# Optimization experiments

Measured on AMD Instinct MI355X. Metric: run time of the kernel, lower is better.

Reference implementation:

```python
import jax, jax.numpy as jnp
import numpy as np

N, H, IN, E = 4096, 64, 64, 10  # notes, hidden, input feat, edge types


def setup_inputs() -> dict:
    key = jax.random.key(0)
    ks = jax.random.split(key, 7)
    std_a = (2.0 / (H + H)) ** 0.5
    std_b = (2.0 / (IN + H)) ** 0.5
    return {
        "input": jax.random.normal(ks[0], (1, N, IN), jnp.float32),
        "hidden": jax.random.normal(ks[1], (1, N, H), jnp.float32),
        # dense per-edge-type adjacency; scaled by 1/N to keep gate pre-activations O(1)
        "edge_matrix": jax.random.uniform(ks[2], (E, N, N), jnp.float32) / N,
        "ba": jnp.zeros((H,), jnp.float32),
        "wz_wr_wh": jax.random.normal(ks[3], (E, H, 3 * H), jnp.float32) * std_a,
        "uz_ur": jax.random.normal(ks[4], (H, 2 * H), jnp.float32) * std_a,
        "uh": jax.random.normal(ks[5], (H, H), jnp.float32) * std_a,
        "input_wzrh": jax.random.normal(ks[6], (IN, 3 * H), jnp.float32) * std_b,
        "iteration": 10,
    }


def reference(input, hidden, edge_matrix, ba, wz_wr_wh, uz_ur, uh, input_wzrh, iteration):
    B, n, _ = input.shape          # B == 1
    h_dim = uh.shape[0]
    n_type = wz_wr_wh.shape[0]
    edge_T = jnp.swapaxes(edge_matrix, 1, 2)          # [E, N, N]
    inp_wzrh = jnp.matmul(input, input_wzrh)          # [B, N, 3H] (loop-invariant)

    def step(h, _):
        # message aggregation per edge type: [E,N,N] @ [B,N,H] -> [E,N,H]
        act = jnp.matmul(edge_T, h) + ba
        # per-edge-type gate projections: [E,N,H] @ [E,H,3H] -> [E,N,3H]
        act_wzrh = jnp.matmul(act, wz_wr_wh) + inp_wzrh
        wz, wr, wh = jnp.split(act_wzrh, 3, axis=-1)
        uz, ur = jnp.split(jnp.matmul(h, uz_ur), 2, axis=-1)  # [B,N,H] each
        z = jax.nn.sigmoid(wz.sum(0) + uz)
        r = jax.nn.sigmoid(wr.sum(0) + ur)
        h_tilde = jnp.tanh(wh.reshape(B, n_type, n, h_dim).sum(1)
                           + jnp.matmul(r * h, uh))
        return (1.0 - z) * h + z * h_tilde, None

    hidden, _ = jax.lax.scan(step, hidden, None, length=iteration)
    return hidden
```

## Files before the change

### kernel.cpp

```cpp
#include <hip/hip_runtime.h>
#include <hip/hip_bf16.h>


typedef __bf16 bf16;
typedef bf16 bf16x8 __attribute__((ext_vector_type(8)));
typedef float f32x4 __attribute__((ext_vector_type(4)));

static_assert(sizeof(bf16) == 2, "bf16 size");

constexpr int kN = 4096;
constexpr int kH = 64;
constexpr int kE = 10;
constexpr int kIter = 10;

constexpr size_t OFF_EDGET = 0;
constexpr size_t SZ_EDGET  = (size_t)kE * kN * kN * 2;
constexpr size_t OFF_HF32  = OFF_EDGET + SZ_EDGET;
constexpr size_t OFF_HBF   = OFF_HF32 + (size_t)kN * kH * 4;
constexpr size_t OFF_HT    = OFF_HBF + (size_t)kN * kH * 2;
constexpr size_t OFF_S     = OFF_HT + (size_t)kN * kH * 2;
constexpr size_t OFF_SBIAS = OFF_S + (size_t)kN * 192 * 4;
constexpr size_t OFF_WT    = OFF_SBIAS + (size_t)kN * 192 * 4;
constexpr size_t OFF_UZT   = OFF_WT + (size_t)kE * 192 * 64 * 2;
constexpr size_t OFF_UHT   = OFF_UZT + (size_t)128 * 64 * 2;
constexpr size_t WS_NEEDED = OFF_UHT + (size_t)64 * 64 * 2;

__device__ __forceinline__ void async16(const void* g, void* l) {
  __builtin_amdgcn_global_load_lds(
      (const __attribute__((address_space(1))) unsigned int*)g,
      (__attribute__((address_space(3))) unsigned int*)l, 16, 0, 0);
}

__device__ __forceinline__ float sigmoidf_(float x) { return 1.0f / (1.0f + __expf(-x)); }
__device__ __forceinline__ float tanhf_(float x) { return 1.0f - 2.0f / (__expf(2.0f * x) + 1.0f); }


__global__ __launch_bounds__(256) void k_transpose(const float* __restrict__ edge,
                                                   bf16* __restrict__ edgeT) {
  const int e = blockIdx.z;
  const int m0 = blockIdx.y * 64;
  const int n0 = blockIdx.x * 64;
  __shared__ bf16 t[64 * 66];
  const float* src = edge + (size_t)e * kN * kN;
  for (int i = threadIdx.x; i < 4096; i += 256) {
    int m = i >> 6, n = i & 63;
    t[n * 66 + m] = (bf16)src[(size_t)(m0 + m) * kN + n0 + n];
  }
  __syncthreads();
  bf16* dst = edgeT + (size_t)e * kN * kN;
  for (int i = threadIdx.x; i < 4096; i += 256) {
    int n = i >> 6, m = i & 63;
    dst[(size_t)(n0 + n) * kN + m0 + m] = t[n * 66 + m];
  }
}

__global__ __launch_bounds__(256) void k_weights(const float* __restrict__ wzwrwh,
                                                 const float* __restrict__ uz_ur,
                                                 const float* __restrict__ uh,
                                                 bf16* __restrict__ WT_all,
                                                 bf16* __restrict__ uzurT,
                                                 bf16* __restrict__ uhT) {
  int idx = blockIdx.x * 256 + threadIdx.x;
  if (idx < kE * 192 * 64) {
    int e = idx / (192 * 64);
    int rem = idx % (192 * 64);
    int c = rem / 64, hh = rem % 64;
    WT_all[idx] = (bf16)wzwrwh[((size_t)e * 64 + hh) * 192 + c];
  }
  if (idx < 128 * 64) {
    int c = idx / 64, hh = idx % 64;
    uzurT[idx] = (bf16)uz_ur[hh * 128 + c];
  }
  if (idx < 64 * 64) {
    int c = idx / 64, hh = idx % 64;
    uhT[idx] = (bf16)uh[hh * 64 + c];
  }
}

__global__ __launch_bounds__(256) void k_hinit(const float* __restrict__ hidden,
                                               float* __restrict__ hf32,
                                               bf16* __restrict__ hbf,
                                               bf16* __restrict__ hT) {
  int idx = blockIdx.x * 256 + threadIdx.x;
  float x = hidden[idx];
  hf32[idx] = x;
  hbf[idx] = (bf16)x;
  int n = idx >> 6, c = idx & 63;
  hT[(size_t)c * kN + n] = (bf16)x;
}

__global__ __launch_bounds__(256) void k_sbias(const float* __restrict__ input,
                                               const float* __restrict__ input_wzrh,
                                               float* __restrict__ SBias,
                                               float* __restrict__ S) {
  int idx = blockIdx.x * 256 + threadIdx.x;
  int n = idx / 192, c = idx % 192;
  float a = 0.f;
#pragma unroll 8
  for (int k = 0; k < 64; k++) a += input[n * 64 + k] * input_wzrh[k * 192 + c];
  a *= (float)kE;
  SBias[idx] = a;
  S[idx] = a;
}

__global__ __launch_bounds__(256) void k_copy(const float* __restrict__ src, float* __restrict__ dst) {
  int idx = blockIdx.x * 256 + threadIdx.x;
  dst[idx] = src[idx];
}

__global__ __launch_bounds__(256, 3) void kA(const bf16* __restrict__ edgeT,
                                             const bf16* __restrict__ hT,
                                             const bf16* __restrict__ WT_all,
                                             const float* __restrict__ ba,
                                             float* __restrict__ S) {
  const int e = blockIdx.y;
  const int n0 = blockIdx.x * 64;
  const int tid = threadIdx.x;
  const int lane = tid & 63;
  const int w = tid >> 6;
  const int l15 = lane & 15;
  const int q = lane >> 4;

  __shared__ bf16 Alds[64 * 64];
  __shared__ bf16 Blds[64 * 64];
  __shared__ bf16 Wlds[192 * 64];
  __shared__ bf16 actlds[64 * 72];

  {
    const int4* src = (const int4*)(WT_all + (size_t)e * 192 * 64);
    int4* dst = (int4*)Wlds;
    for (int i = tid; i < 192 * 64 * 2 / 16; i += 256) dst[i] = src[i];
  }

  f32x4 acc[4] = {};
  const bf16* Abase = edgeT + (size_t)e * kN * kN + (size_t)n0 * kN;

  for (int k0 = 0; k0 < kN; k0 += 64) {
    __syncthreads();
#pragma unroll
    for (int i = 0; i < 2; i++) {
      int c = i * 256 + tid;
      int row = c >> 3, col = (c & 7) * 8;
      async16(Abase + (size_t)row * kN + k0 + col, Alds + c * 8);
    }
#pragma unroll
    for (int i = 0; i < 2; i++) {
      int c = i * 256 + tid;
      int row = c >> 3, col = (c & 7) * 8;
      async16(hT + (size_t)row * kN + k0 + col, Blds + c * 8);
    }
    __syncthreads();
#pragma unroll
    for (int ks = 0; ks < 2; ks++) {
      bf16x8 af = *(const bf16x8*)(Alds + (w * 16 + l15) * 64 + ks * 32 + q * 8);
#pragma unroll
      for (int ct = 0; ct < 4; ct++) {
        bf16x8 bf = *(const bf16x8*)(Blds + (ct * 16 + l15) * 64 + ks * 32 + q * 8);
        acc[ct] = __builtin_amdgcn_mfma_f32_16x16x32_bf16(af, bf, acc[ct], 0, 0, 0);
      }
    }
  }

  __syncthreads();
#pragma unroll
  for (int ct = 0; ct < 4; ct++) {
    int col = ct * 16 + l15;
    float bav = ba[col];
#pragma unroll
    for (int r = 0; r < 4; r++) {
      int row = w * 16 + q * 4 + r;
      actlds[row * 72 + col] = (bf16)(acc[ct][r] + bav);
    }
  }
  __syncthreads();

  f32x4 acc2[12] = {};
#pragma unroll
  for (int ks = 0; ks < 2; ks++) {
    bf16x8 af = *(const bf16x8*)(actlds + (w * 16 + l15) * 72 + ks * 32 + q * 8);
#pragma unroll
    for (int ct = 0; ct < 12; ct++) {
      bf16x8 bf = *(const bf16x8*)(Wlds + (ct * 16 + l15) * 64 + ks * 32 + q * 8);
      acc2[ct] = __builtin_amdgcn_mfma_f32_16x16x32_bf16(af, bf, acc2[ct], 0, 0, 0);
    }
  }
#pragma unroll
  for (int ct = 0; ct < 12; ct++) {
    int col = ct * 16 + l15;
#pragma unroll
    for (int r = 0; r < 4; r++) {
      int row = n0 + w * 16 + q * 4 + r;
      unsafeAtomicAdd(&S[(size_t)row * 192 + col], acc2[ct][r]);
    }
  }
}

__global__ __launch_bounds__(256) void kB(float* __restrict__ S,
                                          const float* __restrict__ SBias,
                                          const bf16* __restrict__ hbf,
                                          const float* __restrict__ hf32,
                                          const bf16* __restrict__ uzurT,
                                          const bf16* __restrict__ uhT,
                                          float* __restrict__ hf32_out,
                                          bf16* __restrict__ hbf_out,
                                          bf16* __restrict__ hT_out,
                                          float* __restrict__ dst) {
  const int n0 = blockIdx.x * 64;
  const int tid = threadIdx.x;
  const int lane = tid & 63;
  const int w = tid >> 6;
  const int l15 = lane & 15;
  const int q = lane >> 4;

  __shared__ bf16 hA[64 * 72];
  __shared__ bf16 uzT[128 * 72];
  __shared__ bf16 uhl[64 * 72];
  __shared__ bf16 rhl[64 * 72];

  for (int i = tid; i < 64 * 8; i += 256) {
    int row = i >> 3, col = (i & 7) * 8;
    *(int4*)(hA + row * 72 + col) = *(const int4*)(hbf + (size_t)(n0 + row) * 64 + col);
  }
  for (int i = tid; i < 128 * 8; i += 256) {
    int row = i >> 3, col = (i & 7) * 8;
    *(int4*)(uzT + row * 72 + col) = *(const int4*)(uzurT + (size_t)row * 64 + col);
  }
  for (int i = tid; i < 64 * 8; i += 256) {
    int row = i >> 3, col = (i & 7) * 8;
    *(int4*)(uhl + row * 72 + col) = *(const int4*)(uhT + (size_t)row * 64 + col);
  }
  __syncthreads();

  f32x4 u[8] = {};
#pragma unroll
  for (int ks = 0; ks < 2; ks++) {
    bf16x8 af = *(const bf16x8*)(hA + (w * 16 + l15) * 72 + ks * 32 + q * 8);
#pragma unroll
    for (int ct = 0; ct < 8; ct++) {
      bf16x8 bf = *(const bf16x8*)(uzT + (ct * 16 + l15) * 72 + ks * 32 + q * 8);
      u[ct] = __builtin_amdgcn_mfma_f32_16x16x32_bf16(af, bf, u[ct], 0, 0, 0);
    }
  }

  float zv[4][4], hv[4][4];
#pragma unroll
  for (int ct = 0; ct < 4; ct++) {
    int col = ct * 16 + l15;
#pragma unroll
    for (int r = 0; r < 4; r++) {
      int row = n0 + w * 16 + q * 4 + r;
      float sz = S[(size_t)row * 192 + col];
      float sr = S[(size_t)row * 192 + 64 + col];
      float z = sigmoidf_(sz + u[ct][r]);
      float rr = sigmoidf_(sr + u[4 + ct][r]);
      float h = hf32[(size_t)row * 64 + col];
      zv[ct][r] = z;
      hv[ct][r] = h;
      rhl[(w * 16 + q * 4 + r) * 72 + col] = (bf16)(rr * h);
    }
  }
  __syncthreads();

  f32x4 t[4] = {};
#pragma unroll
  for (int ks = 0; ks < 2; ks++) {
    bf16x8 af = *(const bf16x8*)(rhl + (w * 16 + l15) * 72 + ks * 32 + q * 8);
#pragma unroll
    for (int ct = 0; ct < 4; ct++) {
      bf16x8 bf = *(const bf16x8*)(uhl + (ct * 16 + l15) * 72 + ks * 32 + q * 8);
      t[ct] = __builtin_amdgcn_mfma_f32_16x16x32_bf16(af, bf, t[ct], 0, 0, 0);
    }
  }

  float hn[4][4];
#pragma unroll
  for (int ct = 0; ct < 4; ct++) {
    int col = ct * 16 + l15;
#pragma unroll
    for (int r = 0; r < 4; r++) {
      int row = n0 + w * 16 + q * 4 + r;
      float wh = S[(size_t)row * 192 + 128 + col];
      float htl = tanhf_(wh + t[ct][r]);
      float z = zv[ct][r];
      float v = (1.0f - z) * hv[ct][r] + z * htl;
      hn[ct][r] = v;
      dst[(size_t)row * 64 + col] = v;
      if (dst != hf32_out) hf32_out[(size_t)row * 64 + col] = v;
      hbf_out[(size_t)row * 64 + col] = (bf16)v;
    }
  }
  __syncthreads();

#pragma unroll
  for (int ct = 0; ct < 4; ct++) {
#pragma unroll
    for (int r = 0; r < 4; r++) {
      int row = w * 16 + q * 4 + r, col = ct * 16 + l15;
      rhl[row * 72 + col] = (bf16)hn[ct][r];
    }
  }
  for (int i = tid; i < 64 * 192; i += 256) S[(size_t)n0 * 192 + i] = SBias[(size_t)n0 * 192 + i];
  __syncthreads();
  for (int i = tid; i < 4096; i += 256) {
    int c = i >> 6, n = i & 63;
    hT_out[(size_t)c * kN + n0 + n] = rhl[n * 72 + c];
  }
}

extern "C" void kernel_launch(void* const* d_in, const int* in_sizes, int n_in,
                              void* d_out, int out_size, void* d_ws, size_t ws_size,
                              hipStream_t stream) {
  const float* input = (const float*)d_in[0];
  const float* hidden = (const float*)d_in[1];
  const float* edge = (const float*)d_in[2];
  const float* ba = (const float*)d_in[3];
  const float* wzwrwh = (const float*)d_in[4];
  const float* uz_ur = (const float*)d_in[5];
  const float* uh = (const float*)d_in[6];
  const float* input_wzrh = (const float*)d_in[7];
  float* out = (float*)d_out;

  if (ws_size < WS_NEEDED) {
    k_copy<<<kN * kH / 256, 256, 0, stream>>>(hidden, out);
    return;
  }

  char* ws = (char*)d_ws;
  bf16* edgeT = (bf16*)(ws + OFF_EDGET);
  float* hf32 = (float*)(ws + OFF_HF32);
  bf16* hbf = (bf16*)(ws + OFF_HBF);
  bf16* hT = (bf16*)(ws + OFF_HT);
  float* S = (float*)(ws + OFF_S);
  float* SBias = (float*)(ws + OFF_SBIAS);
  bf16* WT_all = (bf16*)(ws + OFF_WT);
  bf16* uzurT = (bf16*)(ws + OFF_UZT);
  bf16* uhT = (bf16*)(ws + OFF_UHT);

  k_transpose<<<dim3(kN / 64, kN / 64, kE), 256, 0, stream>>>(edge, edgeT);
  k_weights<<<(kE * 192 * 64) / 256, 256, 0, stream>>>(wzwrwh, uz_ur, uh, WT_all, uzurT, uhT);
  k_hinit<<<(kN * kH) / 256, 256, 0, stream>>>(hidden, hf32, hbf, hT);
  k_sbias<<<(kN * 192) / 256, 256, 0, stream>>>(input, input_wzrh, SBias, S);

  for (int it = 0; it < kIter; it++) {
    kA<<<dim3(kN / 64, kE), 256, 0, stream>>>(edgeT, hT, WT_all, ba, S);
    float* dst = (it == kIter - 1) ? out : hf32;
    kB<<<kN / 64, 256, 0, stream>>>(S, SBias, hbf, hf32, uzurT, uhT, hf32, hbf, hT, dst);
  }
}
```

Baseline: 2.231 ms.

## Double-buffer edge/hidden tiles in kA with XOR-swizzled LDS layout

The main K loop of kA now double-buffers the A (edge) and B (hidden) tiles in LDS, issuing the async loads for the next tile before the MFMAs on the current one. This overlaps global memory traffic with compute and cuts the loop to one barrier per iteration. LDS columns are XOR-swizzled by row to avoid bank conflicts on the bf16x8 reads. The W projection tile is no longer staged in LDS and is read directly from global memory, which frees shared memory for the second buffer but adds uncached-style global reads in the epilogue.

```diff
diff --git a/kernel.cpp b/kernel.cpp
--- a/kernel.cpp
+++ b/kernel.cpp
@@ -121,47 +121,57 @@
   const int l15 = lane & 15;
   const int q = lane >> 4;
 
-  __shared__ bf16 Alds[64 * 64];
-  __shared__ bf16 Blds[64 * 64];
-  __shared__ bf16 Wlds[192 * 64];
+  __shared__ bf16 Alds[2][64 * 64];
+  __shared__ bf16 Blds[2][64 * 64];
   __shared__ bf16 actlds[64 * 72];
 
-  {
-    const int4* src = (const int4*)(WT_all + (size_t)e * 192 * 64);
-    int4* dst = (int4*)Wlds;
-    for (int i = tid; i < 192 * 64 * 2 / 16; i += 256) dst[i] = src[i];
+  const bf16* Abase = edgeT + (size_t)e * kN * kN + (size_t)n0 * kN;
+
+  int srow[2], scol[2];
+#pragma unroll
+  for (int i = 0; i < 2; i++) {
+    int c = i * 256 + tid;
+    srow[i] = c >> 3;
+    scol[i] = ((c & 7) ^ (srow[i] & 7)) * 8;
   }
 
   f32x4 acc[4] = {};
-  const bf16* Abase = edgeT + (size_t)e * kN * kN + (size_t)n0 * kN;
-
+
+#pragma unroll
+  for (int i = 0; i < 2; i++)
+    async16(Abase + (size_t)srow[i] * kN + scol[i], Alds[0] + (i * 256 + tid) * 8);
+#pragma unroll
+  for (int i = 0; i < 2; i++)
+    async16(hT + (size_t)srow[i] * kN + scol[i], Blds[0] + (i * 256 + tid) * 8);
+  __syncthreads();
+
+  int cur = 0;
   for (int k0 = 0; k0 < kN; k0 += 64) {
-    __syncthreads();
-#pragma unroll
-    for (int i = 0; i < 2; i++) {
-      int c = i * 256 + tid;
-      int row = c >> 3, col = (c & 7) * 8;
-      async16(Abase + (size_t)row * kN + k0 + col, Alds + c * 8);
-    }
-#pragma unroll
-    for (int i = 0; i < 2; i++) {
-      int c = i * 256 + tid;
-      int row = c >> 3, col = (c & 7) * 8;
-      async16(hT + (size_t)row * kN + k0 + col, Blds + c * 8);
-    }
-    __syncthreads();
+    if (k0 + 64 < kN) {
+#pragma unroll
+      for (int i = 0; i < 2; i++)
+        async16(Abase + (size_t)srow[i] * kN + (k0 + 64) + scol[i],
+                Alds[cur ^ 1] + (i * 256 + tid) * 8);
+#pragma unroll
+      for (int i = 0; i < 2; i++)
+        async16(hT + (size_t)srow[i] * kN + (k0 + 64) + scol[i],
+                Blds[cur ^ 1] + (i * 256 + tid) * 8);
+    }
 #pragma unroll
     for (int ks = 0; ks < 2; ks++) {
-      bf16x8 af = *(const bf16x8*)(Alds + (w * 16 + l15) * 64 + ks * 32 + q * 8);
+      const int ar = w * 16 + l15;
+      bf16x8 af = *(const bf16x8*)(Alds[cur] + ar * 64 + ((ks * 32 + q * 8) ^ ((ar & 7) << 3)));
 #pragma unroll
       for (int ct = 0; ct < 4; ct++) {
-        bf16x8 bf = *(const bf16x8*)(Blds + (ct * 16 + l15) * 64 + ks * 32 + q * 8);
+        const int br = ct * 16 + l15;
+        bf16x8 bf = *(const bf16x8*)(Blds[cur] + br * 64 + ((ks * 32 + q * 8) ^ ((br & 7) << 3)));
         acc[ct] = __builtin_amdgcn_mfma_f32_16x16x32_bf16(af, bf, acc[ct], 0, 0, 0);
       }
     }
-  }
-
-  __syncthreads();
+    __syncthreads();
+    cur ^= 1;
+  }
+
 #pragma unroll
   for (int ct = 0; ct < 4; ct++) {
     int col = ct * 16 + l15;
@@ -174,13 +184,14 @@
   }
   __syncthreads();
 
+  const bf16* Wg = WT_all + (size_t)e * 192 * 64;
   f32x4 acc2[12] = {};
 #pragma unroll
   for (int ks = 0; ks < 2; ks++) {
     bf16x8 af = *(const bf16x8*)(actlds + (w * 16 + l15) * 72 + ks * 32 + q * 8);
 #pragma unroll
     for (int ct = 0; ct < 12; ct++) {
-      bf16x8 bf = *(const bf16x8*)(Wlds + (ct * 16 + l15) * 64 + ks * 32 + q * 8);
+      bf16x8 bf = *(const bf16x8*)(Wg + (ct * 16 + l15) * 64 + ks * 32 + q * 8);
       acc2[ct] = __builtin_amdgcn_mfma_f32_16x16x32_bf16(af, bf, acc2[ct], 0, 0, 0);
     }
   }
```

After: 2.264 ms. About the same (+1.5%).

## Move per-edge gate projection into kB and load kA operands directly to registers

Applied to the files above, without the earlier changes.

The per-edge-type projection of aggregated messages, previously done in kA with fp32 atomics into S, is moved into kB. kA now writes a bf16 per-edge act buffer, and kB sums the projections over all edge types in registers before adding SBias. This removes the atomics and the per-iteration reset of S. kA also drops the LDS staging and barriers in favour of direct global-to-register loads with double-buffered prefetch. The trade-offs are redundant hT loads across waves without LDS sharing, more serial MFMA work in kB, which has only 64 blocks, and an extra act buffer written and read each iteration.

```diff
diff --git a/kernel.cpp b/kernel.cpp
--- a/kernel.cpp
+++ b/kernel.cpp
@@ -18,18 +18,12 @@
 constexpr size_t OFF_HF32  = OFF_EDGET + SZ_EDGET;
 constexpr size_t OFF_HBF   = OFF_HF32 + (size_t)kN * kH * 4;
 constexpr size_t OFF_HT    = OFF_HBF + (size_t)kN * kH * 2;
-constexpr size_t OFF_S     = OFF_HT + (size_t)kN * kH * 2;
-constexpr size_t OFF_SBIAS = OFF_S + (size_t)kN * 192 * 4;
+constexpr size_t OFF_ACT   = OFF_HT + (size_t)kN * kH * 2;
+constexpr size_t OFF_SBIAS = OFF_ACT + (size_t)kE * kN * 64 * 2;
 constexpr size_t OFF_WT    = OFF_SBIAS + (size_t)kN * 192 * 4;
 constexpr size_t OFF_UZT   = OFF_WT + (size_t)kE * 192 * 64 * 2;
 constexpr size_t OFF_UHT   = OFF_UZT + (size_t)128 * 64 * 2;
 constexpr size_t WS_NEEDED = OFF_UHT + (size_t)64 * 64 * 2;
-
-__device__ __forceinline__ void async16(const void* g, void* l) {
-  __builtin_amdgcn_global_load_lds(
-      (const __attribute__((address_space(1))) unsigned int*)g,
-      (__attribute__((address_space(3))) unsigned int*)l, 16, 0, 0);
-}
 
 __device__ __forceinline__ float sigmoidf_(float x) { return 1.0f / (1.0f + __expf(-x)); }
 __device__ __forceinline__ float tanhf_(float x) { return 1.0f - 2.0f / (__expf(2.0f * x) + 1.0f); }
@@ -91,16 +85,13 @@
 
 __global__ __launch_bounds__(256) void k_sbias(const float* __restrict__ input,
                                                const float* __restrict__ input_wzrh,
-                                               float* __restrict__ SBias,
-                                               float* __restrict__ S) {
+                                               float* __restrict__ SBias) {
   int idx = blockIdx.x * 256 + threadIdx.x;
   int n = idx / 192, c = idx % 192;
   float a = 0.f;
 #pragma unroll 8
   for (int k = 0; k < 64; k++) a += input[n * 64 + k] * input_wzrh[k * 192 + c];
-  a *= (float)kE;
-  SBias[idx] = a;
-  S[idx] = a;
+  SBias[idx] = a * (float)kE;
 }
 
 __global__ __launch_bounds__(256) void k_copy(const float* __restrict__ src, float* __restrict__ dst) {
@@ -108,11 +99,10 @@
   dst[idx] = src[idx];
 }
 
-__global__ __launch_bounds__(256, 3) void kA(const bf16* __restrict__ edgeT,
-                                             const bf16* __restrict__ hT,
-                                             const bf16* __restrict__ WT_all,
-                                             const float* __restrict__ ba,
-                                             float* __restrict__ S) {
+__global__ __launch_bounds__(256) void kA(const bf16* __restrict__ edgeT,
+                                          const bf16* __restrict__ hT,
+                                          const float* __restrict__ ba,
+                                          bf16* __restrict__ actAll) {
   const int e = blockIdx.y;
   const int n0 = blockIdx.x * 64;
   const int tid = threadIdx.x;
@@ -121,81 +111,68 @@
   const int l15 = lane & 15;
   const int q = lane >> 4;
 
-  __shared__ bf16 Alds[64 * 64];
-  __shared__ bf16 Blds[64 * 64];
-  __shared__ bf16 Wlds[192 * 64];
   __shared__ bf16 actlds[64 * 72];
 
-  {
-    const int4* src = (const int4*)(WT_all + (size_t)e * 192 * 64);
-    int4* dst = (int4*)Wlds;
-    for (int i = tid; i < 192 * 64 * 2 / 16; i += 256) dst[i] = src[i];
-  }
+  const bf16* aRow = edgeT + (size_t)e * kN * kN + (size_t)(n0 + w * 16 + l15) * kN + q * 8;
+  const bf16* bRow0 = hT + (size_t)(0 * 16 + l15) * kN + q * 8;
+  const bf16* bRow1 = hT + (size_t)(1 * 16 + l15) * kN + q * 8;
+  const bf16* bRow2 = hT + (size_t)(2 * 16 + l15) * kN + q * 8;
+  const bf16* bRow3 = hT + (size_t)(3 * 16 + l15) * kN + q * 8;
 
   f32x4 acc[4] = {};
-  const bf16* Abase = edgeT + (size_t)e * kN * kN + (size_t)n0 * kN;
-
-  for (int k0 = 0; k0 < kN; k0 += 64) {
-    __syncthreads();
-#pragma unroll
-    for (int i = 0; i < 2; i++) {
-      int c = i * 256 + tid;
-      int row = c >> 3, col = (c & 7) * 8;
-      async16(Abase + (size_t)row * kN + k0 + col, Alds + c * 8);
-    }
-#pragma unroll
-    for (int i = 0; i < 2; i++) {
-      int c = i * 256 + tid;
-      int row = c >> 3, col = (c & 7) * 8;
-      async16(hT + (size_t)row * kN + k0 + col, Blds + c * 8);
-    }
-    __syncthreads();
-#pragma unroll
-    for (int ks = 0; ks < 2; ks++) {
-      bf16x8 af = *(const bf16x8*)(Alds + (w * 16 + l15) * 64 + ks * 32 + q * 8);
-#pragma unroll
-      for (int ct = 0; ct < 4; ct++) {
-        bf16x8 bf = *(const bf16x8*)(Blds + (ct * 16 + l15) * 64 + ks * 32 + q * 8);
-        acc[ct] = __builtin_amdgcn_mfma_f32_16x16x32_bf16(af, bf, acc[ct], 0, 0, 0);
-      }
-    }
-  }
-
-  __syncthreads();
+
+  bf16x8 a0[2], a1[2];
+  bf16x8 b0[2][4], b1[2][4];
+
+#define LOADK(K0, A, B)                                    \
+  {                                                        \
+    _Pragma("unroll") for (int ks = 0; ks < 2; ks++) {     \
+      int ko = (K0) + ks * 32;                             \
+      A[ks] = *(const bf16x8*)(aRow + ko);                 \
+      B[ks][0] = *(const bf16x8*)(bRow0 + ko);             \
+      B[ks][1] = *(const bf16x8*)(bRow1 + ko);             \
+      B[ks][2] = *(const bf16x8*)(bRow2 + ko);             \
+      B[ks][3] = *(const bf16x8*)(bRow3 + ko);             \
+    }                                                      \
+  }
+#define MFMAK(A, B)                                                                        \
+  {                                                                                        \
+    _Pragma("unroll") for (int ks = 0; ks < 2; ks++) {                                     \
+      _Pragma("unroll") for (int ct = 0; ct < 4; ct++) {                                   \
+        acc[ct] = __builtin_amdgcn_mfma_f32_16x16x32_bf16(A[ks], B[ks][ct], acc[ct], 0, 0, 0); \
+      }                                                                                    \
+    }                                                                                      \
+  }
+
+  LOADK(0, a0, b0)
+  for (int k0 = 0; k0 < kN; k0 += 128) {
+    LOADK(k0 + 64, a1, b1)
+    MFMAK(a0, b0)
+    if (k0 + 128 < kN) LOADK(k0 + 128, a0, b0)
+    MFMAK(a1, b1)
+  }
+#undef LOADK
+#undef MFMAK
+
 #pragma unroll
   for (int ct = 0; ct < 4; ct++) {
     int col = ct * 16 + l15;
     float bav = ba[col];
 #pragma unroll
     for (int r = 0; r < 4; r++) {
-      int row = w * 16 + q * 4 + r;
-      actlds[row * 72 + col] = (bf16)(acc[ct][r] + bav);
-    }
-  }
-  __syncthreads();
-
-  f32x4 acc2[12] = {};
-#pragma unroll
-  for (int ks = 0; ks < 2; ks++) {
-    bf16x8 af = *(const bf16x8*)(actlds + (w * 16 + l15) * 72 + ks * 32 + q * 8);
-#pragma unroll
-    for (int ct = 0; ct < 12; ct++) {
-      bf16x8 bf = *(const bf16x8*)(Wlds + (ct * 16 + l15) * 64 + ks * 32 + q * 8);
-      acc2[ct] = __builtin_amdgcn_mfma_f32_16x16x32_bf16(af, bf, acc2[ct], 0, 0, 0);
-    }
-  }
-#pragma unroll
-  for (int ct = 0; ct < 12; ct++) {
-    int col = ct * 16 + l15;
-#pragma unroll
-    for (int r = 0; r < 4; r++) {
-      int row = n0 + w * 16 + q * 4 + r;
-      unsafeAtomicAdd(&S[(size_t)row * 192 + col], acc2[ct][r]);
-    }
-  }
-}
-
-__global__ __launch_bounds__(256) void kB(float* __restrict__ S,
+      actlds[(w * 16 + q * 4 + r) * 72 + col] = (bf16)(acc[ct][r] + bav);
+    }
+  }
+  __syncthreads();
+  bf16* dstp = actAll + ((size_t)e * kN + n0) * 64;
+  for (int i = tid; i < 512; i += 256) {
+    int row = i >> 3, col = (i & 7) * 8;
+    *(int4*)(dstp + (size_t)row * 64 + col) = *(const int4*)(actlds + row * 72 + col);
+  }
+}
+
+__global__ __launch_bounds__(256) void kB(const bf16* __restrict__ actAll,
+                                          const bf16* __restrict__ WT_all,
                                           const float* __restrict__ SBias,
                                           const bf16* __restrict__ hbf,
                                           const float* __restrict__ hf32,
@@ -229,6 +206,25 @@
     int row = i >> 3, col = (i & 7) * 8;
     *(int4*)(uhl + row * 72 + col) = *(const int4*)(uhT + (size_t)row * 64 + col);
   }
+
+  f32x4 acc2[12] = {};
+  {
+    const bf16* aBase = actAll + (size_t)(n0 + w * 16 + l15) * 64 + q * 8;
+    const bf16* wBase = WT_all + (size_t)l15 * 64 + q * 8;
+    for (int e = 0; e < kE; e++) {
+      const bf16* ap = aBase + (size_t)e * kN * 64;
+      const bf16* wp = wBase + (size_t)e * 192 * 64;
+#pragma unroll
+      for (int ks = 0; ks < 2; ks++) {
+        bf16x8 af = *(const bf16x8*)(ap + ks * 32);
+#pragma unroll
+        for (int ct = 0; ct < 12; ct++) {
+          bf16x8 bf = *(const bf16x8*)(wp + ct * 16 * 64 + ks * 32);
+          acc2[ct] = __builtin_amdgcn_mfma_f32_16x16x32_bf16(af, bf, acc2[ct], 0, 0, 0);
+        }
+      }
+    }
+  }
   __syncthreads();
 
   f32x4 u[8] = {};
@@ -249,8 +245,8 @@
 #pragma unroll
     for (int r = 0; r < 4; r++) {
       int row = n0 + w * 16 + q * 4 + r;
-      float sz = S[(size_t)row * 192 + col];
-      float sr = S[(size_t)row * 192 + 64 + col];
+      float sz = SBias[(size_t)row * 192 + col] + acc2[ct][r];
+      float sr = SBias[(size_t)row * 192 + 64 + col] + acc2[4 + ct][r];
       float z = sigmoidf_(sz + u[ct][r]);
       float rr = sigmoidf_(sr + u[4 + ct][r]);
       float h = hf32[(size_t)row * 64 + col];
@@ -279,7 +275,7 @@
 #pragma unroll
     for (int r = 0; r < 4; r++) {
       int row = n0 + w * 16 + q * 4 + r;
-      float wh = S[(size_t)row * 192 + 128 + col];
+      float wh = SBias[(size_t)row * 192 + 128 + col] + acc2[8 + ct][r];
       float htl = tanhf_(wh + t[ct][r]);
       float z = zv[ct][r];
       float v = (1.0f - z) * hv[ct][r] + z * htl;
@@ -299,7 +295,6 @@
       rhl[row * 72 + col] = (bf16)hn[ct][r];
     }
   }
-  for (int i = tid; i < 64 * 192; i += 256) S[(size_t)n0 * 192 + i] = SBias[(size_t)n0 * 192 + i];
   __syncthreads();
   for (int i = tid; i < 4096; i += 256) {
     int c = i >> 6, n = i & 63;
@@ -330,7 +325,7 @@
   float* hf32 = (float*)(ws + OFF_HF32);
   bf16* hbf = (bf16*)(ws + OFF_HBF);
   bf16* hT = (bf16*)(ws + OFF_HT);
-  float* S = (float*)(ws + OFF_S);
+  bf16* actAll = (bf16*)(ws + OFF_ACT);
   float* SBias = (float*)(ws + OFF_SBIAS);
   bf16* WT_all = (bf16*)(ws + OFF_WT);
   bf16* uzurT = (bf16*)(ws + OFF_UZT);
@@ -339,11 +334,12 @@
   k_transpose<<<dim3(kN / 64, kN / 64, kE), 256, 0, stream>>>(edge, edgeT);
   k_weights<<<(kE * 192 * 64) / 256, 256, 0, stream>>>(wzwrwh, uz_ur, uh, WT_all, uzurT, uhT);
   k_hinit<<<(kN * kH) / 256, 256, 0, stream>>>(hidden, hf32, hbf, hT);
-  k_sbias<<<(kN * 192) / 256, 256, 0, stream>>>(input, input_wzrh, SBias, S);
+  k_sbias<<<(kN * 192) / 256, 256, 0, stream>>>(input, input_wzrh, SBias);
 
   for (int it = 0; it < kIter; it++) {
-    kA<<<dim3(kN / 64, kE), 256, 0, stream>>>(edgeT, hT, WT_all, ba, S);
+    kA<<<dim3(kN / 64, kE), 256, 0, stream>>>(edgeT, hT, ba, actAll);
     float* dst = (it == kIter - 1) ? out : hf32;
-    kB<<<kN / 64, 256, 0, stream>>>(S, SBias, hbf, hf32, uzurT, uhT, hf32, hbf, hT, dst);
-  }
-}
+    kB<<<kN / 64, 256, 0, stream>>>(actAll, WT_all, SBias, hbf, hf32, uzurT, uhT,
+                                    hf32, hbf, hT, dst);
+  }
+}
```

Measured after the change: 3.697 ms. 65.7% more time.
